# Performance work log

Measured on AMD Instinct MI355X. Metric: run time of the kernel, lower is better.

Reference implementation:

```python
import jax, jax.numpy as jnp
import numpy as np

TOP_K = 2  # num_experts_per_tok


def setup_inputs() -> dict:
    key = jax.random.key(0)
    ks = jax.random.split(key, 5)
    B, S, D, M, E = 4, 2048, 2048, 2048, 8
    x = jax.random.normal(ks[0], (B, S, D), dtype=jnp.float32)
    gate_kernel = jax.random.normal(ks[1], (D, E), dtype=jnp.float32) / np.sqrt(D)
    wi_0 = jax.random.normal(ks[2], (E, D, M), dtype=jnp.float32) / np.sqrt(D)
    wi_1 = jax.random.normal(ks[3], (E, D, M), dtype=jnp.float32) / np.sqrt(D)
    wo = jax.random.normal(ks[4], (E, M, D), dtype=jnp.float32) / np.sqrt(M)
    return {"x": x, "gate_kernel": gate_kernel, "wi_0": wi_0, "wi_1": wi_1, "wo": wo}


def reference(x, gate_kernel, wi_0, wi_1, wo):
    E = gate_kernel.shape[-1]
    # Gate logits: (B, S, E)
    gate_logits = jnp.einsum("bsd,de->bse", x, gate_kernel)
    # Top-k routing, then softmax over the selected experts' logits
    top_k_weights, top_k_indices = jax.lax.top_k(gate_logits, TOP_K)
    top_k_weights = jax.nn.softmax(top_k_weights.astype(jnp.float32), axis=-1).astype(x.dtype)
    # Dense combine weights per expert: (B, S, E)
    combine_w = jnp.sum(
        jax.nn.one_hot(top_k_indices, E, dtype=x.dtype) * top_k_weights[..., None], axis=-2
    )
    # Grouped GEMM (dense-masked form, as in MaxText dense_matmul path)
    h0 = jnp.einsum("bsd,edm->bsem", x, wi_0)  # (B, S, E, M)
    h1 = jnp.einsum("bsd,edm->bsem", x, wi_1)
    h = jax.nn.silu(h0) * h1 * combine_w[..., None]
    out = jnp.einsum("bsem,emd->bsd", h, wo)  # (B, S, D)
    return out
```

## Files before the change

### kernel.cpp

```cpp
#include <hip/hip_runtime.h>
#include <hip/hip_bf16.h>
#include <stdint.h>

#define TT   8192
#define DD   2048
#define MM   2048
#define NE   8

typedef float f32x4 __attribute__((ext_vector_type(4)));
typedef short s16x8 __attribute__((ext_vector_type(8)));
typedef unsigned int u32;

static __device__ __forceinline__ short f2bf(float f) {
  __hip_bfloat16 h = __float2bfloat16(f);
  short s;
  __builtin_memcpy(&s, &h, 2);
  return s;
}

static __device__ __forceinline__ void gload_lds16(const short* g, short* lds) {
  __builtin_amdgcn_global_load_lds(
      (const __attribute__((address_space(1))) u32*)g,
      (__attribute__((address_space(3))) u32*)lds, 16, 0, 0);
}

__global__ __launch_bounds__(256) void tcvt_kernel(
    const float* __restrict__ w0, const float* __restrict__ w1, const float* __restrict__ w2,
    short* __restrict__ o0, short* __restrict__ o1, short* __restrict__ o2) {
  __shared__ short tile[64][65];
  const int bz = blockIdx.z;
  const float* in; short* out;
  if (bz < 8)       { in = w0; out = o0; }
  else if (bz < 16) { in = w1; out = o1; }
  else              { in = w2; out = o2; }
  const int ex = bz & 7;
  const float* src = in + (size_t)ex * DD * MM;
  short* dst = out + (size_t)ex * DD * MM;
  const int r0 = blockIdx.y * 64;
  const int c0 = blockIdx.x * 64;
  const int t = threadIdx.x;
  const int rr = t >> 4, cc = (t & 15) * 4;
  #pragma unroll
  for (int i = 0; i < 4; i++) {
    int row = rr + i * 16;
    f32x4 v = *(const f32x4*)(src + (size_t)(r0 + row) * MM + c0 + cc);
    tile[cc + 0][row] = f2bf(v[0]);
    tile[cc + 1][row] = f2bf(v[1]);
    tile[cc + 2][row] = f2bf(v[2]);
    tile[cc + 3][row] = f2bf(v[3]);
  }
  __syncthreads();
  const int orow = t >> 2, c8 = (t & 3) * 16;
  s16x8 v0, v1;
  #pragma unroll
  for (int i = 0; i < 8; i++) { v0[i] = tile[orow][c8 + i]; v1[i] = tile[orow][c8 + 8 + i]; }
  short* dp = dst + (size_t)(c0 + orow) * DD + r0 + c8;
  *(s16x8*)(dp) = v0;
  *(s16x8*)(dp + 8) = v1;
}

__global__ __launch_bounds__(256) void gate_kernel(const float* __restrict__ x,
    const float* __restrict__ gk, int* __restrict__ counts,
    int* __restrict__ tkidx, float* __restrict__ tkw, short* __restrict__ xbf) {
  int t = blockIdx.x;
  const float* xr = x + (size_t)t * DD;
  const int d0 = threadIdx.x * 8;
  f32x4 a = *(const f32x4*)(xr + d0);
  f32x4 b = *(const f32x4*)(xr + d0 + 4);
  s16x8 v;
  v[0]=f2bf(a[0]); v[1]=f2bf(a[1]); v[2]=f2bf(a[2]); v[3]=f2bf(a[3]);
  v[4]=f2bf(b[0]); v[5]=f2bf(b[1]); v[6]=f2bf(b[2]); v[7]=f2bf(b[3]);
  *(s16x8*)(xbf + (size_t)t * DD + d0) = v;

  float acc[NE];
  #pragma unroll
  for (int e = 0; e < NE; e++) acc[e] = 0.f;
  #pragma unroll
  for (int j = 0; j < 8; j++) {
    float xv = (j < 4) ? a[j] : b[j - 4];
    const float* g = gk + (size_t)(d0 + j) * NE;
    #pragma unroll
    for (int e = 0; e < NE; e++) acc[e] += xv * g[e];
  }
  #pragma unroll
  for (int e = 0; e < NE; e++) {
    #pragma unroll
    for (int off = 32; off >= 1; off >>= 1)
      acc[e] += __shfl_xor(acc[e], off, 64);
  }
  __shared__ float red[4][NE];
  int wid = threadIdx.x >> 6;
  int lane = threadIdx.x & 63;
  if (lane == 0) {
    #pragma unroll
    for (int e = 0; e < NE; e++) red[wid][e] = acc[e];
  }
  __syncthreads();
  if (threadIdx.x == 0) {
    float l[NE];
    #pragma unroll
    for (int e = 0; e < NE; e++) l[e] = red[0][e] + red[1][e] + red[2][e] + red[3][e];
    int i1 = 0; float v1 = l[0];
    #pragma unroll
    for (int e = 1; e < NE; e++) if (l[e] > v1) { v1 = l[e]; i1 = e; }
    int i2 = -1; float v2 = -1e30f;
    #pragma unroll
    for (int e = 0; e < NE; e++) if (e != i1 && l[e] > v2) { v2 = l[e]; i2 = e; }
    float p = __expf(v2 - v1);
    float inv = 1.f / (1.f + p);
    tkidx[t*2]   = i1; tkidx[t*2+1] = i2;
    tkw[t*2]     = inv; tkw[t*2+1]  = p * inv;
    atomicAdd(&counts[i1], 1);
    atomicAdd(&counts[i2], 1);
  }
}

__global__ __launch_bounds__(256) void scatter_kernel(const int* __restrict__ counts,
    int* __restrict__ offsets, const int* __restrict__ tkidx,
    const float* __restrict__ tkw, int* __restrict__ ltok, float* __restrict__ lwt,
    int* __restrict__ slots) {
  __shared__ int soff[NE];
  __shared__ int scur[NE];
  if (threadIdx.x == 0) {
    int s = 0;
    for (int e = 0; e < NE; e++) { offsets[e] = s; soff[e] = s; s += counts[e]; scur[e] = 0; }
    offsets[NE] = s;
  }
  __syncthreads();
  for (int i = threadIdx.x; i < TT * 2; i += 256) {
    int e = tkidx[i];
    int pos = atomicAdd(&scur[e], 1);
    int dst = soff[e] + pos;
    ltok[dst] = i >> 1;
    lwt[dst]  = tkw[i];
    slots[i]  = dst;
  }
}

__global__ __launch_bounds__(256) void combine_kernel(const float* __restrict__ comb,
    const int* __restrict__ slots, float* __restrict__ out) {
  const int t = blockIdx.x;
  const int s0 = slots[2 * t], s1 = slots[2 * t + 1];
  const f32x4* p0 = (const f32x4*)(comb + (size_t)s0 * DD);
  const f32x4* p1 = (const f32x4*)(comb + (size_t)s1 * DD);
  f32x4* po = (f32x4*)(out + (size_t)t * DD);
  #pragma unroll
  for (int i = 0; i < 2; i++) {
    int idx = threadIdx.x + i * 256;
    po[idx] = p0[idx] + p1[idx];
  }
}

__device__ __forceinline__ void find_seg(const int* __restrict__ offsets, int tile, int bm,
                                         int& e, int& row0, int& rows, int& seg) {
  e = -1; row0 = 0; rows = 0; seg = 0;
  int accT = 0, prev = offsets[0];
  #pragma unroll
  for (int i = 0; i < NE; i++) {
    int nxt = offsets[i+1];
    int cnt = nxt - prev;
    int nt = (cnt + bm - 1) / bm;
    if (e < 0 && tile < accT + nt) { e = i; row0 = (tile - accT) * bm; rows = cnt; seg = prev; }
    accT += nt; prev = nxt;
  }
}

__device__ __forceinline__ void xcd_map(int& tile, int& nyi) {
  const int nx = gridDim.x;
  const int nwg = nx * gridDim.y;
  const int bid = blockIdx.y * nx + blockIdx.x;
  const int cpx = nwg >> 3;
  const int s = (bid & 7) * cpx + (bid >> 3);
  tile = s % nx;
  nyi  = s / nx;
}

#define MAXT_F 136

__global__ __launch_bounds__(256, 2) void gemm1_fast(
    const short* __restrict__ xbf,
    const short* __restrict__ w0t, const short* __restrict__ w1t,
    const int* __restrict__ offsets,
    const int* __restrict__ ltok, const float* __restrict__ lwt,
    short* __restrict__ hbuf) {
  __shared__ short As[128 * 64];
  __shared__ short B0s[128 * 64];
  __shared__ short B1s[128 * 64];
  __shared__ float w_s[128];

  int tile, nyi;
  xcd_map(tile, nyi);
  const int n0 = nyi * 128;
  int e, row0, rows, seg;
  find_seg(offsets, tile, 128, e, row0, rows, seg);
  if (e < 0) return;

  const int tid = threadIdx.x;
  const int lane = tid & 63, wid = tid >> 6;
  if (tid < 128) {
    int gr = row0 + tid;
    w_s[tid] = (gr < rows) ? lwt[seg + gr] : 0.f;
  }

  const int swz = ((lane & 7) ^ (lane >> 3)) * 8;
  const short* abase[4];
  const short* b0base[4];
  const short* b1base[4];
  #pragma unroll
  for (int c = 0; c < 4; c++) {
    int chunk = wid * 4 + c;
    int r = chunk * 8 + (lane >> 3);
    int gr = row0 + r; if (gr >= rows) gr = rows - 1;
    int tok = ltok[seg + gr];
    abase[c]  = xbf + (size_t)tok * DD + swz;
    int n = n0 + r;
    b0base[c] = w0t + ((size_t)e * MM + n) * DD + swz;
    b1base[c] = w1t + ((size_t)e * MM + n) * DD + swz;
  }

  const int wr = wid >> 1, wc = wid & 1;
  const int lr = lane & 15;
  const int kq = (lane >> 4) * 8;

  f32x4 acc0[4][4], acc1[4][4];
  #pragma unroll
  for (int i = 0; i < 4; i++)
    #pragma unroll
    for (int j = 0; j < 4; j++) { acc0[i][j] = 0.f; acc1[i][j] = 0.f; }

  for (int k0 = 0; k0 < DD; k0 += 64) {
    #pragma unroll
    for (int c = 0; c < 4; c++) {
      int chunk = wid * 4 + c;
      gload_lds16(abase[c]  + k0, As  + chunk * 512);
      gload_lds16(b0base[c] + k0, B0s + chunk * 512);
      gload_lds16(b1base[c] + k0, B1s + chunk * 512);
    }
    __syncthreads();

    #pragma unroll
    for (int ks = 0; ks < 2; ks++) {
      s16x8 a[4], b0[4], b1[4];
      #pragma unroll
      for (int mi = 0; mi < 4; mi++) {
        int row = wr * 64 + mi * 16 + lr;
        int koff = (ks * 32 + kq) ^ ((row & 7) * 8);
        a[mi] = *(const s16x8*)&As[row * 64 + koff];
      }
      #pragma unroll
      for (int ni = 0; ni < 4; ni++) {
        int row = wc * 64 + ni * 16 + lr;
        int koff = (ks * 32 + kq) ^ ((row & 7) * 8);
        b0[ni] = *(const s16x8*)&B0s[row * 64 + koff];
        b1[ni] = *(const s16x8*)&B1s[row * 64 + koff];
      }
      #pragma unroll
      for (int mi = 0; mi < 4; mi++)
        #pragma unroll
        for (int ni = 0; ni < 4; ni++) {
          acc0[mi][ni] = __builtin_amdgcn_mfma_f32_16x16x32_bf16(a[mi], b0[ni], acc0[mi][ni], 0, 0, 0);
          acc1[mi][ni] = __builtin_amdgcn_mfma_f32_16x16x32_bf16(a[mi], b1[ni], acc1[mi][ni], 0, 0, 0);
        }
    }
    __syncthreads();
  }

  const int lq = lane >> 4;
  #pragma unroll
  for (int mi = 0; mi < 4; mi++) {
    #pragma unroll
    for (int jj = 0; jj < 4; jj++) {
      int r = wr * 64 + mi * 16 + lq * 4 + jj;
      int gr = row0 + r;
      if (gr < rows) {
        float wgt = w_s[r];
        size_t hrow = (size_t)(seg + gr) * MM + n0;
        #pragma unroll
        for (int ni = 0; ni < 4; ni++) {
          int c = wc * 64 + ni * 16 + lr;
          float g = acc0[mi][ni][jj];
          float u = acc1[mi][ni][jj];
          float act = g / (1.f + __expf(-g));
          hbuf[hrow + c] = f2bf(act * u * wgt);
        }
      }
    }
  }
}

__global__ __launch_bounds__(256, 2) void gemm2_fast(
    const short* __restrict__ hbuf,
    const short* __restrict__ wot,
    const int* __restrict__ offsets,
    float* __restrict__ comb) {
  __shared__ short As[128 * 64];
  __shared__ short B0s[128 * 64];
  __shared__ short B1s[128 * 64];

  int tile, nyi;
  xcd_map(tile, nyi);
  const int n0 = nyi * 256;
  int e, row0, rows, seg;
  find_seg(offsets, tile, 128, e, row0, rows, seg);
  if (e < 0) return;

  const int tid = threadIdx.x;
  const int lane = tid & 63, wid = tid >> 6;

  const int swz = ((lane & 7) ^ (lane >> 3)) * 8;
  const short* abase[4];
  const short* b0base[4];
  const short* b1base[4];
  #pragma unroll
  for (int c = 0; c < 4; c++) {
    int chunk = wid * 4 + c;
    int r = chunk * 8 + (lane >> 3);
    int gr = row0 + r; if (gr >= rows) gr = rows - 1;
    abase[c] = hbuf + (size_t)(seg + gr) * MM + swz;
    b0base[c] = wot + ((size_t)e * DD + n0 + r) * MM + swz;
    b1base[c] = wot + ((size_t)e * DD + n0 + 128 + r) * MM + swz;
  }

  const int wr = wid >> 1, wc = wid & 1;
  const int lr = lane & 15;
  const int kq = (lane >> 4) * 8;

  f32x4 acc0[4][4], acc1[4][4];
  #pragma unroll
  for (int i = 0; i < 4; i++)
    #pragma unroll
    for (int j = 0; j < 4; j++) { acc0[i][j] = 0.f; acc1[i][j] = 0.f; }

  for (int k0 = 0; k0 < MM; k0 += 64) {
    #pragma unroll
    for (int c = 0; c < 4; c++) {
      int chunk = wid * 4 + c;
      gload_lds16(abase[c]  + k0, As  + chunk * 512);
      gload_lds16(b0base[c] + k0, B0s + chunk * 512);
      gload_lds16(b1base[c] + k0, B1s + chunk * 512);
    }
    __syncthreads();

    #pragma unroll
    for (int ks = 0; ks < 2; ks++) {
      s16x8 a[4], b0[4], b1[4];
      #pragma unroll
      for (int mi = 0; mi < 4; mi++) {
        int row = wr * 64 + mi * 16 + lr;
        int koff = (ks * 32 + kq) ^ ((row & 7) * 8);
        a[mi] = *(const s16x8*)&As[row * 64 + koff];
      }
      #pragma unroll
      for (int ni = 0; ni < 4; ni++) {
        int row = wc * 64 + ni * 16 + lr;
        int koff = (ks * 32 + kq) ^ ((row & 7) * 8);
        b0[ni] = *(const s16x8*)&B0s[row * 64 + koff];
        b1[ni] = *(const s16x8*)&B1s[row * 64 + koff];
      }
      #pragma unroll
      for (int mi = 0; mi < 4; mi++)
        #pragma unroll
        for (int ni = 0; ni < 4; ni++) {
          acc0[mi][ni] = __builtin_amdgcn_mfma_f32_16x16x32_bf16(a[mi], b0[ni], acc0[mi][ni], 0, 0, 0);
          acc1[mi][ni] = __builtin_amdgcn_mfma_f32_16x16x32_bf16(a[mi], b1[ni], acc1[mi][ni], 0, 0, 0);
        }
    }
    __syncthreads();
  }

  const int lq = lane >> 4;
  #pragma unroll
  for (int mi = 0; mi < 4; mi++) {
    #pragma unroll
    for (int jj = 0; jj < 4; jj++) {
      int r = wr * 64 + mi * 16 + lq * 4 + jj;
      int gr = row0 + r;
      if (gr < rows) {
        size_t orow = (size_t)(seg + gr) * DD + n0;
        #pragma unroll
        for (int ni = 0; ni < 4; ni++) {
          int c = wc * 64 + ni * 16 + lr;
          comb[orow + c] = acc0[mi][ni][jj];
          comb[orow + 128 + c] = acc1[mi][ni][jj];
        }
      }
    }
  }
}

extern "C" void kernel_launch(void* const* d_in, const int* in_sizes, int n_in,
                              void* d_out, int out_size, void* d_ws, size_t ws_size,
                              hipStream_t stream) {
  const float* x   = (const float*)d_in[0];
  const float* gk  = (const float*)d_in[1];
  const float* wi0 = (const float*)d_in[2];
  const float* wi1 = (const float*)d_in[3];
  const float* wo  = (const float*)d_in[4];
  float* out = (float*)d_out;

  char* w = (char*)d_ws;
  int*   counts  = (int*)(w);
  int*   offsets = (int*)(w + 256);
  int*   tkidx   = (int*)(w + 1024);
  float* tkw     = (float*)(w + 1024 + 65536);
  int*   ltok    = (int*)(w + 1024 + 2*65536);
  float* lwt     = (float*)(w + 1024 + 3*65536);
  int*   slots   = (int*)(w + 1024 + 4*65536);
  short* xbf  = (short*)(w + 524288);
  short* hbuf = xbf + (size_t)TT * DD;
  short* w0t  = hbuf + (size_t)2 * TT * MM;
  short* w1t  = w0t + (size_t)NE * DD * MM;
  short* wot  = w1t + (size_t)NE * DD * MM;
  float* comb = (float*)w0t;

  hipMemsetAsync(counts, 0, 64, stream);

  gate_kernel<<<TT, 256, 0, stream>>>(x, gk, counts, tkidx, tkw, xbf);
  scatter_kernel<<<1, 256, 0, stream>>>(counts, offsets, tkidx, tkw, ltok, lwt, slots);
  tcvt_kernel<<<dim3(MM/64, DD/64, 24), 256, 0, stream>>>(wi0, wi1, wo, w0t, w1t, wot);

  gemm1_fast<<<dim3(MAXT_F, MM/128), 256, 0, stream>>>(xbf, w0t, w1t, offsets, ltok, lwt, hbuf);
  gemm2_fast<<<dim3(MAXT_F, DD/256), 256, 0, stream>>>(hbuf, wot, offsets, comb);
  combine_kernel<<<TT, 256, 0, stream>>>(comb, slots, out);
}
```

Before: 904.0 us.

## Parallelize scatter per expert, remap XCD tiles, shrink gemm2 M-tile to 64

```diff
diff --git a/kernel.cpp b/kernel.cpp
--- a/kernel.cpp
+++ b/kernel.cpp
@@ -10,6 +10,7 @@
 typedef float f32x4 __attribute__((ext_vector_type(4)));
 typedef short s16x8 __attribute__((ext_vector_type(8)));
 typedef unsigned int u32;
+typedef unsigned long long u64;
 
 static __device__ __forceinline__ short f2bf(float f) {
   __hip_bfloat16 h = __float2bfloat16(f);
@@ -119,21 +120,45 @@
     int* __restrict__ offsets, const int* __restrict__ tkidx,
     const float* __restrict__ tkw, int* __restrict__ ltok, float* __restrict__ lwt,
     int* __restrict__ slots) {
-  __shared__ int soff[NE];
-  __shared__ int scur[NE];
-  if (threadIdx.x == 0) {
+  const int e = blockIdx.x;
+  const int tid = threadIdx.x;
+  const int wid = tid >> 6, lane = tid & 63;
+  __shared__ int base_s;
+  __shared__ int wsum[4];
+  if (tid == 0) {
     int s = 0;
-    for (int e = 0; e < NE; e++) { offsets[e] = s; soff[e] = s; s += counts[e]; scur[e] = 0; }
-    offsets[NE] = s;
+    #pragma unroll
+    for (int i = 0; i < NE; i++) {
+      if (e == 0) offsets[i] = s;
+      if (i < e) s += counts[i];
+      else if (e == 0) s += counts[i];
+    }
+    if (e == 0) offsets[NE] = s;
+    int bs = 0;
+    for (int i = 0; i < e; i++) bs += counts[i];
+    base_s = bs;
   }
   __syncthreads();
-  for (int i = threadIdx.x; i < TT * 2; i += 256) {
-    int e = tkidx[i];
-    int pos = atomicAdd(&scur[e], 1);
-    int dst = soff[e] + pos;
-    ltok[dst] = i >> 1;
-    lwt[dst]  = tkw[i];
-    slots[i]  = dst;
+  int base = base_s;
+  for (int it = 0; it < (TT * 2) / 256; it++) {
+    int i = it * 256 + tid;
+    bool m = (tkidx[i] == e);
+    u64 b = __ballot(m);
+    if (lane == 0) wsum[wid] = __popcll(b);
+    __syncthreads();
+    int pre = 0;
+    #pragma unroll
+    for (int w = 0; w < 4; w++) if (w < wid) pre += wsum[w];
+    int tot = wsum[0] + wsum[1] + wsum[2] + wsum[3];
+    int rank = __popcll(b & ((lane == 0) ? 0ull : ((1ull << lane) - 1ull)));
+    if (m) {
+      int dst = base + pre + rank;
+      ltok[dst] = i >> 1;
+      lwt[dst]  = tkw[i];
+      slots[i]  = dst;
+    }
+    __syncthreads();
+    base += tot;
   }
 }
 
@@ -165,17 +190,15 @@
   }
 }
 
-__device__ __forceinline__ void xcd_map(int& tile, int& nyi) {
-  const int nx = gridDim.x;
-  const int nwg = nx * gridDim.y;
-  const int bid = blockIdx.y * nx + blockIdx.x;
-  const int cpx = nwg >> 3;
-  const int s = (bid & 7) * cpx + (bid >> 3);
-  tile = s % nx;
-  nyi  = s / nx;
-}
-
-#define MAXT_F 136
+__device__ __forceinline__ void xcd_map(int ypx, int& tile, int& nyi) {
+  const int bid = blockIdx.y * gridDim.x + blockIdx.x;
+  const int xcd = bid & 7;
+  const int i = bid >> 3;
+  tile = i / ypx;
+  nyi  = xcd * ypx + (i % ypx);
+}
+
+#define MAXT1 136
 
 __global__ __launch_bounds__(256, 2) void gemm1_fast(
     const short* __restrict__ xbf,
@@ -189,7 +212,7 @@
   __shared__ float w_s[128];
 
   int tile, nyi;
-  xcd_map(tile, nyi);
+  xcd_map(2, tile, nyi);
   const int n0 = nyi * 128;
   int e, row0, rows, seg;
   find_seg(offsets, tile, 128, e, row0, rows, seg);
@@ -288,35 +311,42 @@
   }
 }
 
+#define MAXT2 264
+
 __global__ __launch_bounds__(256, 2) void gemm2_fast(
     const short* __restrict__ hbuf,
     const short* __restrict__ wot,
     const int* __restrict__ offsets,
     float* __restrict__ comb) {
-  __shared__ short As[128 * 64];
+  __shared__ short As[64 * 64];
   __shared__ short B0s[128 * 64];
   __shared__ short B1s[128 * 64];
 
   int tile, nyi;
-  xcd_map(tile, nyi);
+  xcd_map(1, tile, nyi);
   const int n0 = nyi * 256;
   int e, row0, rows, seg;
-  find_seg(offsets, tile, 128, e, row0, rows, seg);
+  find_seg(offsets, tile, 64, e, row0, rows, seg);
   if (e < 0) return;
 
   const int tid = threadIdx.x;
   const int lane = tid & 63, wid = tid >> 6;
 
   const int swz = ((lane & 7) ^ (lane >> 3)) * 8;
-  const short* abase[4];
+  const short* abase[2];
+  #pragma unroll
+  for (int c = 0; c < 2; c++) {
+    int chunk = wid * 2 + c;
+    int r = chunk * 8 + (lane >> 3);
+    int gr = row0 + r; if (gr >= rows) gr = rows - 1;
+    abase[c] = hbuf + (size_t)(seg + gr) * MM + swz;
+  }
   const short* b0base[4];
   const short* b1base[4];
   #pragma unroll
   for (int c = 0; c < 4; c++) {
     int chunk = wid * 4 + c;
     int r = chunk * 8 + (lane >> 3);
-    int gr = row0 + r; if (gr >= rows) gr = rows - 1;
-    abase[c] = hbuf + (size_t)(seg + gr) * MM + swz;
     b0base[c] = wot + ((size_t)e * DD + n0 + r) * MM + swz;
     b1base[c] = wot + ((size_t)e * DD + n0 + 128 + r) * MM + swz;
   }
@@ -325,17 +355,21 @@
   const int lr = lane & 15;
   const int kq = (lane >> 4) * 8;
 
-  f32x4 acc0[4][4], acc1[4][4];
-  #pragma unroll
-  for (int i = 0; i < 4; i++)
+  f32x4 acc0[2][4], acc1[2][4];
+  #pragma unroll
+  for (int i = 0; i < 2; i++)
     #pragma unroll
     for (int j = 0; j < 4; j++) { acc0[i][j] = 0.f; acc1[i][j] = 0.f; }
 
   for (int k0 = 0; k0 < MM; k0 += 64) {
+    #pragma unroll
+    for (int c = 0; c < 2; c++) {
+      int chunk = wid * 2 + c;
+      gload_lds16(abase[c] + k0, As + chunk * 512);
+    }
     #pragma unroll
     for (int c = 0; c < 4; c++) {
       int chunk = wid * 4 + c;
-      gload_lds16(abase[c]  + k0, As  + chunk * 512);
       gload_lds16(b0base[c] + k0, B0s + chunk * 512);
       gload_lds16(b1base[c] + k0, B1s + chunk * 512);
     }
@@ -343,10 +377,10 @@
 
     #pragma unroll
     for (int ks = 0; ks < 2; ks++) {
-      s16x8 a[4], b0[4], b1[4];
-      #pragma unroll
-      for (int mi = 0; mi < 4; mi++) {
-        int row = wr * 64 + mi * 16 + lr;
+      s16x8 a[2], b0[4], b1[4];
+      #pragma unroll
+      for (int mi = 0; mi < 2; mi++) {
+        int row = wr * 32 + mi * 16 + lr;
         int koff = (ks * 32 + kq) ^ ((row & 7) * 8);
         a[mi] = *(const s16x8*)&As[row * 64 + koff];
       }
@@ -358,7 +392,7 @@
         b1[ni] = *(const s16x8*)&B1s[row * 64 + koff];
       }
       #pragma unroll
-      for (int mi = 0; mi < 4; mi++)
+      for (int mi = 0; mi < 2; mi++)
         #pragma unroll
         for (int ni = 0; ni < 4; ni++) {
           acc0[mi][ni] = __builtin_amdgcn_mfma_f32_16x16x32_bf16(a[mi], b0[ni], acc0[mi][ni], 0, 0, 0);
@@ -370,10 +404,10 @@
 
   const int lq = lane >> 4;
   #pragma unroll
-  for (int mi = 0; mi < 4; mi++) {
+  for (int mi = 0; mi < 2; mi++) {
     #pragma unroll
     for (int jj = 0; jj < 4; jj++) {
-      int r = wr * 64 + mi * 16 + lq * 4 + jj;
+      int r = wr * 32 + mi * 16 + lq * 4 + jj;
       int gr = row0 + r;
       if (gr < rows) {
         size_t orow = (size_t)(seg + gr) * DD + n0;
@@ -416,10 +450,10 @@
   hipMemsetAsync(counts, 0, 64, stream);
 
   gate_kernel<<<TT, 256, 0, stream>>>(x, gk, counts, tkidx, tkw, xbf);
-  scatter_kernel<<<1, 256, 0, stream>>>(counts, offsets, tkidx, tkw, ltok, lwt, slots);
+  scatter_kernel<<<NE, 256, 0, stream>>>(counts, offsets, tkidx, tkw, ltok, lwt, slots);
   tcvt_kernel<<<dim3(MM/64, DD/64, 24), 256, 0, stream>>>(wi0, wi1, wo, w0t, w1t, wot);
 
-  gemm1_fast<<<dim3(MAXT_F, MM/128), 256, 0, stream>>>(xbf, w0t, w1t, offsets, ltok, lwt, hbuf);
-  gemm2_fast<<<dim3(MAXT_F, DD/256), 256, 0, stream>>>(hbuf, wot, offsets, comb);
+  gemm1_fast<<<dim3(MAXT1, MM/128), 256, 0, stream>>>(xbf, w0t, w1t, offsets, ltok, lwt, hbuf);
+  gemm2_fast<<<dim3(MAXT2, DD/256), 256, 0, stream>>>(hbuf, wot, offsets, comb);
   combine_kernel<<<TT, 256, 0, stream>>>(comb, slots, out);
 }
```

New measurement: 904.8 us. Within noise of the previous version (+0.1%).
